# Optimization experiments

Measured on AMD Instinct MI355X. Metric: run time of the kernel, lower is better.

## Reference

```python
import jax, jax.numpy as jnp
import numpy as np

SCALE = 1.0 / np.sqrt(2.0).astype(np.float32)  # 1/sqrt(head_dim=2)


def setup_inputs() -> dict:
    key = jax.random.key(0)
    k1, k2 = jax.random.split(key)
    shape = (1, 2048, 8, 2)  # (batch, seq_len, heads, spinor_dim=2)
    return {
        "spinors_real": jax.random.normal(k1, shape, dtype=jnp.float32),
        "spinors_imag": jax.random.normal(k2, shape, dtype=jnp.float32),
    }


def reference(spinors_real, spinors_imag):
    # assemble complex spinors (batch, seq, heads, 2)
    spinors = jax.lax.complex(spinors_real, spinors_imag)
    # L2 norm over the spinor dim (real-valued magnitude norm, as torch.norm on cfloat)
    nrm = jnp.sqrt(jnp.sum(spinors_real * spinors_real + spinors_imag * spinors_imag,
                           axis=-1, keepdims=True))
    normed = spinors / nrm
    # Hermitian inner product logits: (b, i, j, h)
    logits = jnp.einsum('bihd,bjhd->bijh', jnp.conj(normed), normed)
    # softmax over key axis j of the real part, scaled
    attn = jax.nn.softmax(logits.real * SCALE, axis=2)
    # combine original (unnormalized) spinors
    out = jnp.einsum('bijh,bjhd->bihd', attn.astype(spinors.dtype), spinors)
    return out
```

## Files before the change

kernel.cpp:

```cpp
#include <hip/hip_runtime.h>


#define S 2048
#define H 8
#define QR 8

__device__ inline float fast_exp2(float x) {
#if __has_builtin(__builtin_amdgcn_exp2f)
    return __builtin_amdgcn_exp2f(x);
#else
    return exp2f(x);
#endif
}

__global__ __launch_bounds__(256) void su2_prep(const float* __restrict__ re,
                                                const float* __restrict__ im,
                                                float4* __restrict__ kv,
                                                float4* __restrict__ vv) {
    int t = blockIdx.x * 256 + threadIdx.x;
    int h = t >> 11;
    int j = t & 2047;
    int src = (j * H + h) * 2;
    float r0 = re[src], r1 = re[src + 1];
    float i0 = im[src], i1 = im[src + 1];
    float ss = r0 * r0 + i0 * i0 + r1 * r1 + i1 * i1;
    float inv = rsqrtf(ss);
    kv[t] = make_float4(r0 * inv, i0 * inv, r1 * inv, i1 * inv);
    vv[t] = make_float4(r0, i0, r1, i1);
}

__global__ __launch_bounds__(256) void su2_attn(const float4* __restrict__ kv,
                                                const float4* __restrict__ vv,
                                                float2* __restrict__ outr,
                                                float2* __restrict__ outi) {
    const int h    = blockIdx.y;
    const int lane = threadIdx.x & 63;
    const int wave = threadIdx.x >> 6;
    const int i_base = (blockIdx.x * 4 + wave) * QR;

    const float4* __restrict__ kvh = kv + (h << 11);
    const float4* __restrict__ vvh = vv + (h << 11);

    float4 q[QR];
#pragma unroll
    for (int r = 0; r < QR; ++r) q[r] = kvh[i_base + r];

    float  l[QR];
    float4 acc[QR];
#pragma unroll
    for (int r = 0; r < QR; ++r) {
        l[r] = 0.f;
        acc[r] = make_float4(0.f, 0.f, 0.f, 0.f);
    }

    const float c = 0.70710678118654752440f * 1.44269504088896340736f;

#pragma unroll 4
    for (int jj = 0; jj < S / 64; ++jj) {
        int j = jj * 64 + lane;
        float4 k = kvh[j];
        float4 v = vvh[j];
#pragma unroll
        for (int r = 0; r < QR; ++r) {
            float d = q[r].x * k.x + q[r].y * k.y + q[r].z * k.z + q[r].w * k.w;
            float p = fast_exp2(d * c);
            l[r] += p;
            acc[r].x += p * v.x;
            acc[r].y += p * v.y;
            acc[r].z += p * v.z;
            acc[r].w += p * v.w;
        }
    }

#pragma unroll
    for (int r = 0; r < QR; ++r) {
#pragma unroll
        for (int m = 32; m >= 1; m >>= 1) {
            l[r]     += __shfl_xor(l[r], m, 64);
            acc[r].x += __shfl_xor(acc[r].x, m, 64);
            acc[r].y += __shfl_xor(acc[r].y, m, 64);
            acc[r].z += __shfl_xor(acc[r].z, m, 64);
            acc[r].w += __shfl_xor(acc[r].w, m, 64);
        }
    }

    if (lane == 0) {
#pragma unroll
        for (int r = 0; r < QR; ++r) {
            float inv = 1.0f / l[r];
            int i = i_base + r;
            outr[i * H + h] = make_float2(acc[r].x * inv, acc[r].z * inv);
            outi[i * H + h] = make_float2(acc[r].y * inv, acc[r].w * inv);
        }
    }
}

extern "C" void kernel_launch(void* const* d_in, const int* in_sizes, int n_in,
                              void* d_out, int out_size, void* d_ws, size_t ws_size,
                              hipStream_t stream) {
    const float* re = (const float*)d_in[0];
    const float* im = (const float*)d_in[1];
    float4* kv = (float4*)d_ws;
    float4* vv = kv + S * H;
    float2* outr = (float2*)d_out;
    float2* outi = outr + S * H;

    su2_prep<<<dim3(64), dim3(256), 0, stream>>>(re, im, kv, vv);
    su2_attn<<<dim3(S / 32, H), dim3(256), 0, stream>>>(kv, vv, outr, outi);
}
```

Measured before the change: 75.71 us.

## Share unnormalized key/value table and use packed float2 FMAs in attention loop

```diff
diff --git a/kernel.cpp b/kernel.cpp
--- a/kernel.cpp
+++ b/kernel.cpp
@@ -12,25 +12,31 @@
     return exp2f(x);
 #endif
 }
+__device__ inline float2 f2mul(float2 a, float2 b) {
+    return make_float2(a.x * b.x, a.y * b.y);
+}
+__device__ inline float2 f2fma(float2 a, float2 b, float2 c) {
+    return make_float2(fmaf(a.x, b.x, c.x), fmaf(a.y, b.y, c.y));
+}
 
 __global__ __launch_bounds__(256) void su2_prep(const float* __restrict__ re,
                                                 const float* __restrict__ im,
-                                                float4* __restrict__ kv,
-                                                float4* __restrict__ vv) {
+                                                float4* __restrict__ vtab,
+                                                float* __restrict__ ntab) {
     int t = blockIdx.x * 256 + threadIdx.x;
     int h = t >> 11;
     int j = t & 2047;
-    int src = (j * H + h) * 2;
-    float r0 = re[src], r1 = re[src + 1];
-    float i0 = im[src], i1 = im[src + 1];
-    float ss = r0 * r0 + i0 * i0 + r1 * r1 + i1 * i1;
-    float inv = rsqrtf(ss);
-    kv[t] = make_float4(r0 * inv, i0 * inv, r1 * inv, i1 * inv);
-    vv[t] = make_float4(r0, i0, r1, i1);
+    const float2* re2 = (const float2*)re;
+    const float2* im2 = (const float2*)im;
+    float2 r = re2[j * H + h];
+    float2 m = im2[j * H + h];
+    float ss = r.x * r.x + m.x * m.x + r.y * r.y + m.y * m.y;
+    vtab[t] = make_float4(r.x, m.x, r.y, m.y);
+    ntab[t] = rsqrtf(ss);
 }
 
-__global__ __launch_bounds__(256) void su2_attn(const float4* __restrict__ kv,
-                                                const float4* __restrict__ vv,
+__global__ __launch_bounds__(256) void su2_attn(const float4* __restrict__ vtab,
+                                                const float* __restrict__ ntab,
                                                 float2* __restrict__ outr,
                                                 float2* __restrict__ outi) {
     const int h    = blockIdx.y;
@@ -38,37 +44,44 @@
     const int wave = threadIdx.x >> 6;
     const int i_base = (blockIdx.x * 4 + wave) * QR;
 
-    const float4* __restrict__ kvh = kv + (h << 11);
-    const float4* __restrict__ vvh = vv + (h << 11);
+    const float4* __restrict__ vt = vtab + (h << 11);
+    const float*  __restrict__ nt = ntab + (h << 11);
 
-    float4 q[QR];
+    const float c = 0.70710678118654752440f * 1.44269504088896340736f;
+
+    float2 qc0[QR], qc1[QR];
 #pragma unroll
-    for (int r = 0; r < QR; ++r) q[r] = kvh[i_base + r];
+    for (int r = 0; r < QR; ++r) {
+        float4 v = vt[i_base + r];
+        float  s = nt[i_base + r] * c;
+        qc0[r] = make_float2(v.x * s, v.y * s);
+        qc1[r] = make_float2(v.z * s, v.w * s);
+    }
 
     float  l[QR];
-    float4 acc[QR];
+    float2 a0[QR], a1[QR];
 #pragma unroll
     for (int r = 0; r < QR; ++r) {
-        l[r] = 0.f;
-        acc[r] = make_float4(0.f, 0.f, 0.f, 0.f);
+        l[r]  = 0.f;
+        a0[r] = make_float2(0.f, 0.f);
+        a1[r] = make_float2(0.f, 0.f);
     }
-
-    const float c = 0.70710678118654752440f * 1.44269504088896340736f;
 
 #pragma unroll 4
     for (int jj = 0; jj < S / 64; ++jj) {
         int j = jj * 64 + lane;
-        float4 k = kvh[j];
-        float4 v = vvh[j];
+        float4 v   = vt[j];
+        float  inv = nt[j];
+        float2 v0 = make_float2(v.x, v.y);
+        float2 v1 = make_float2(v.z, v.w);
 #pragma unroll
         for (int r = 0; r < QR; ++r) {
-            float d = q[r].x * k.x + q[r].y * k.y + q[r].z * k.z + q[r].w * k.w;
-            float p = fast_exp2(d * c);
+            float2 d2 = f2fma(qc1[r], v1, f2mul(qc0[r], v0));
+            float  p  = fast_exp2((d2.x + d2.y) * inv);
             l[r] += p;
-            acc[r].x += p * v.x;
-            acc[r].y += p * v.y;
-            acc[r].z += p * v.z;
-            acc[r].w += p * v.w;
+            float2 pp = make_float2(p, p);
+            a0[r] = f2fma(pp, v0, a0[r]);
+            a1[r] = f2fma(pp, v1, a1[r]);
         }
     }
 
@@ -76,21 +89,21 @@
     for (int r = 0; r < QR; ++r) {
 #pragma unroll
         for (int m = 32; m >= 1; m >>= 1) {
-            l[r]     += __shfl_xor(l[r], m, 64);
-            acc[r].x += __shfl_xor(acc[r].x, m, 64);
-            acc[r].y += __shfl_xor(acc[r].y, m, 64);
-            acc[r].z += __shfl_xor(acc[r].z, m, 64);
-            acc[r].w += __shfl_xor(acc[r].w, m, 64);
+            l[r]    += __shfl_xor(l[r], m, 64);
+            a0[r].x += __shfl_xor(a0[r].x, m, 64);
+            a0[r].y += __shfl_xor(a0[r].y, m, 64);
+            a1[r].x += __shfl_xor(a1[r].x, m, 64);
+            a1[r].y += __shfl_xor(a1[r].y, m, 64);
         }
     }
 
     if (lane == 0) {
 #pragma unroll
         for (int r = 0; r < QR; ++r) {
-            float inv = 1.0f / l[r];
+            float invl = 1.0f / l[r];
             int i = i_base + r;
-            outr[i * H + h] = make_float2(acc[r].x * inv, acc[r].z * inv);
-            outi[i * H + h] = make_float2(acc[r].y * inv, acc[r].w * inv);
+            outr[i * H + h] = make_float2(a0[r].x * invl, a1[r].x * invl);
+            outi[i * H + h] = make_float2(a0[r].y * invl, a1[r].y * invl);
         }
     }
 }
@@ -100,11 +113,11 @@
                               hipStream_t stream) {
     const float* re = (const float*)d_in[0];
     const float* im = (const float*)d_in[1];
-    float4* kv = (float4*)d_ws;
-    float4* vv = kv + S * H;
+    float4* vtab = (float4*)d_ws;
+    float*  ntab = (float*)(vtab + S * H);
     float2* outr = (float2*)d_out;
     float2* outi = outr + S * H;
 
-    su2_prep<<<dim3(64), dim3(256), 0, stream>>>(re, im, kv, vv);
-    su2_attn<<<dim3(S / 32, H), dim3(256), 0, stream>>>(kv, vv, outr, outi);
+    su2_prep<<<dim3(64), dim3(256), 0, stream>>>(re, im, vtab, ntab);
+    su2_attn<<<dim3(S / 32, H), dim3(256), 0, stream>>>(vtab, ntab, outr, outi);
 }
```

After: 77.71 us. +2.6%, slower.
